# Optimization experiments

Hardware: AMD Instinct MI355X
Metric: run time of the kernel (lower is better)

## Reference

```python
import jax, jax.numpy as jnp
import numpy as np

P, C, NX, NY, NT = 2, 1, 128, 128, 8


def setup_inputs() -> dict:
    key = jax.random.key(0)
    k1, k2 = jax.random.split(key)
    x_5D = jax.random.normal(k1, (P, C, NX, NY, NT), dtype=jnp.float32)
    # per-pixel regularization parameter map (positive)
    lambda_reg = jax.random.uniform(k2, (P, 1, NX, NY, NT), dtype=jnp.float32) * 0.1 + 1e-3
    ten = jnp.asarray(10.0, jnp.float32)  # nn.Parameter init value 10.0
    return {"x_5D": x_5D, "lambda_reg": lambda_reg, "tau": ten, "sigma": ten,
            "theta": ten, "T": 128}


def _grad_G(u):
    # u: (P,1,Nx,Ny,Nt) -> forward finite differences with circular boundary,
    # stacked over the 3 spatial/temporal dims: (P,3,Nx,Ny,Nt)
    v = u[:, 0]
    return jnp.stack([jnp.roll(v, -1, axis=a) - v for a in (1, 2, 3)], axis=1)


def _grad_GH(q):
    # adjoint of _grad_G (negative divergence): (P,3,Nx,Ny,Nt) -> (P,1,Nx,Ny,Nt)
    out = sum(jnp.roll(q[:, d], 1, axis=d + 1) - q[:, d] for d in range(3))
    return out[:, None]


def _clip_act(q, lam):
    # pointwise projection onto [-lam, lam] ball: q * lam / max(lam, |q|)
    return q * lam / jnp.maximum(lam, jnp.abs(q))


def reference(x_5D, lambda_reg, tau, sigma, theta, T):
    dtype = x_5D.dtype
    # L = sqrt(op_norm_AHA^2 + op_norm_GHG^2) = sqrt(1 + 12)
    L = jnp.sqrt(jnp.asarray(13.0, dtype))
    sig = jax.nn.sigmoid(sigma).astype(dtype) / L
    tau_ = jax.nn.sigmoid(tau).astype(dtype) / L
    th = jax.nn.sigmoid(theta).astype(dtype)

    xnoisy = x_5D
    x0 = x_5D
    xbar = x_5D
    p = x_5D
    q = jnp.zeros((x_5D.shape[0], 3) + x_5D.shape[2:], dtype=dtype)

    def step(carry, _):
        x0, xbar, p, q = carry
        p = (p + sig * (xbar - xnoisy)) / (1.0 + sig)
        q = _clip_act(q + sig * _grad_G(xbar), lambda_reg)
        x1 = x0 - tau_ * p - tau_ * _grad_GH(q)
        # updating xbar on the final iteration is dead code in the original
        # (it only skips unused work), so a uniform scan is mathematically identical
        xbar = x1 + th * (x1 - x0)
        return (x1, xbar, p, q), None

    (x1, _, _, _), _ = jax.lax.scan(step, (x0, xbar, p, q), None, length=T)
    return x1
```

## Files before the change

### kernel.cpp

```cpp
#include <hip/hip_runtime.h>
#include <math.h>

#define NSITES (2 * 128 * 128 * 8)
#define NBLK   256
#define NSUP   32
#define TLX    16
#define TLY    24
#define NCOL   (TLX * TLY)
#define NTHR   (NCOL * 2)

union F4 { float4 v; float f[4]; };
union U4 { uint4 v; unsigned w[4]; };

__device__ __forceinline__ unsigned pk_bf2(float lo, float hi) {
    unsigned r;
    asm("v_cvt_pk_bf16_f32 %0, %1, %2" : "=v"(r) : "v"(lo), "v"(hi));
    return r;
}
__device__ __forceinline__ float bf_lo(unsigned p) { return __uint_as_float(p << 16); }
__device__ __forceinline__ float bf_hi(unsigned p) { return __uint_as_float(p & 0xFFFF0000u); }

__device__ __forceinline__ float dpp_swap1(float x) {
    return __int_as_float(
        __builtin_amdgcn_mov_dpp(__float_as_int(x), 0xB1, 0xF, 0xF, true));
}

template <bool FIRST, bool LAST>
__global__ __launch_bounds__(NTHR, 3) void pdhg_col(
    const float* __restrict__ x,
    const float* __restrict__ lam,
    const float* __restrict__ tau_p,
    const float* __restrict__ sigma_p,
    const float* __restrict__ theta_p,
    const unsigned long long* __restrict__ inD1,
    const unsigned long long* __restrict__ inD2,
    unsigned long long* __restrict__ outD1,
    unsigned long long* __restrict__ outD2,
    float* __restrict__ out_final)
{
    __shared__ float4 Lxb[2][NTHR];
    __shared__ uint4  Lqq[2][NTHR];

    const int b  = 32 * (blockIdx.x & 7) + (blockIdx.x >> 3);
    const int pp = b >> 7;
    const int rr = b & 127;
    const int bx = rr >> 3;
    const int by = rr & 7;

    const int t   = threadIdx.x;
    const int tm  = t & 1;
    const int col = t >> 1;
    const int lx  = col / TLY;
    const int ly  = col - lx * TLY;

    const int X  = ((bx << 3) + lx - 4) & 127;
    const int Y  = ((by << 4) + ly - 4) & 127;
    const int Xm = (X + 127) & 127;
    const int Ym = (Y + 127) & 127;

    const int gcol = (pp << 17) | (X << 10) | (Y << 3);
    const int gxm  = (pp << 17) | (Xm << 10) | (Y << 3);
    const int gym  = (pp << 17) | (X << 10) | (Ym << 3);

    const bool comp = (lx >= 1) && (lx < 15) && (ly >= 1) && (ly < 23);

    const float L = 3.605551275463989f;
    const float s_sig = (1.f / (1.f + __expf(-sigma_p[0]))) / L;
    const float s_tau = (1.f / (1.f + __expf(-tau_p[0]))) / L;
    const float s_th  =  1.f / (1.f + __expf(-theta_p[0]));
    const float inv1s = 1.f / (1.f + s_sig);

    const int c4 = (gcol >> 2) + tm;

    float xn[4], lamc[4], lamx[4], lamy[4];
    {
        const float4* x4 = (const float4*)x;
        const float4* l4 = (const float4*)lam;
        if (FIRST || comp) {
            F4 a; a.v = x4[c4];
            #pragma unroll
            for (int j = 0; j < 4; ++j) xn[j] = a.f[j];
        } else {
            #pragma unroll
            for (int j = 0; j < 4; ++j) xn[j] = 0.f;
        }
        if (comp) {
            F4 a;
            a.v = l4[c4];
            #pragma unroll
            for (int j = 0; j < 4; ++j) lamc[j] = a.f[j];
            a.v = l4[(gxm >> 2) + tm];
            #pragma unroll
            for (int j = 0; j < 4; ++j) lamx[j] = a.f[j];
            a.v = l4[(gym >> 2) + tm];
            #pragma unroll
            for (int j = 0; j < 4; ++j) lamy[j] = a.f[j];
        } else {
            #pragma unroll
            for (int j = 0; j < 4; ++j) { lamc[j] = 0.f; lamx[j] = 0.f; lamy[j] = 0.f; }
        }
    }
    const float lamtm = dpp_swap1(lamc[3]);

    float x0[4], p[4], q0[4], q1[4], q2[4], xb[4];
    if (FIRST) {
        #pragma unroll
        for (int j = 0; j < 4; ++j) {
            const float v = xn[j];
            x0[j] = v; p[j] = v; xb[j] = v;
            q0[j] = 0.f; q1[j] = 0.f; q2[j] = 0.f;
        }
    } else {
        const uint4* d1 = (const uint4*)inD1;
        const int base = (gcol >> 1) + 2 * tm;
        #pragma unroll
        for (int k = 0; k < 2; ++k) {
            U4 a; a.v = d1[base + k];
            #pragma unroll
            for (int m = 0; m < 2; ++m) {
                const int j = 2 * k + m;
                const unsigned lo = a.w[2 * m], hi = a.w[2 * m + 1];
                xb[j] = bf_lo(lo); q0[j] = bf_hi(lo);
                q1[j] = bf_lo(hi); q2[j] = bf_hi(hi);
            }
        }
        if (comp) {
            const float4* d2 = (const float4*)inD2;
            #pragma unroll
            for (int k = 0; k < 2; ++k) {
                F4 a; a.v = d2[base + k];
                p[2 * k]     = a.f[0]; x0[2 * k]     = a.f[1];
                p[2 * k + 1] = a.f[2]; x0[2 * k + 1] = a.f[3];
            }
        } else {
            #pragma unroll
            for (int j = 0; j < 4; ++j) { p[j] = 0.f; x0[j] = 0.f; }
        }
    }

    auto clip = [](float v, float l) { return __builtin_amdgcn_fmed3f(v, -l, l); };

    auto substep = [&](const int h) {
        const int pb = h & 1;
        if (lx >= 3 - h && lx < 13 + h && ly >= 3 - h && ly < 21 + h) {
            Lxb[pb][t] = make_float4(xb[0], xb[1], xb[2], xb[3]);
            U4 w;
            w.w[0] = pk_bf2(q0[0], q1[0]); w.w[1] = pk_bf2(q0[1], q1[1]);
            w.w[2] = pk_bf2(q0[2], q1[2]); w.w[3] = pk_bf2(q0[3], q1[3]);
            Lqq[pb][t] = w.v;
        }
        __syncthreads();
        if (lx >= 4 - h && lx < 12 + h && ly >= 4 - h && ly < 20 + h) {
            const float xb_tp = dpp_swap1(xb[0]);
            const float xb_tm = dpp_swap1(xb[3]);
            const float q2_tm = dpp_swap1(q2[3]);
            F4 xp, xm, yp, ym; U4 qx, qy;
            xp.v = Lxb[pb][t + 2 * TLY];
            xm.v = Lxb[pb][t - 2 * TLY];
            yp.v = Lxb[pb][t + 2];
            ym.v = Lxb[pb][t - 2];
            qx.v = Lqq[pb][t - 2 * TLY];
            qy.v = Lqq[pb][t - 2];
            float oxb[4], oq2[4];
            #pragma unroll
            for (int j = 0; j < 4; ++j) { oxb[j] = xb[j]; oq2[j] = q2[j]; }
            #pragma unroll
            for (int j = 0; j < 4; ++j) {
                const float ob   = oxb[j];
                const float xbtp = (j < 3) ? oxb[j + 1] : xb_tp;
                const float xbtm = (j > 0) ? oxb[j - 1] : xb_tm;
                const float q2tm = (j > 0) ? oq2[j - 1] : q2_tm;
                const float lT   = (j > 0) ? lamc[j - 1] : lamtm;
                const float pn  = (p[j] + s_sig * (ob - xn[j])) * inv1s;
                const float q0n = clip(q0[j] + s_sig * (xp.f[j] - ob), lamc[j]);
                const float q1n = clip(q1[j] + s_sig * (yp.f[j] - ob), lamc[j]);
                const float q2n = clip(oq2[j] + s_sig * (xbtp - ob), lamc[j]);
                const float q0m = clip(bf_lo(qx.w[j]) + s_sig * (ob - xm.f[j]), lamx[j]);
                const float q1m = clip(bf_hi(qy.w[j]) + s_sig * (ob - ym.f[j]), lamy[j]);
                const float q2m = clip(q2tm + s_sig * (ob - xbtm), lT);
                const float dv  = (q0m - q0n) + (q1m - q1n) + (q2m - q2n);
                const float x1  = x0[j] - s_tau * (pn + dv);
                xb[j] = x1 + s_th * (x1 - x0[j]);
                x0[j] = x1; p[j] = pn;
                q0[j] = q0n; q1[j] = q1n; q2[j] = q2n;
            }
        }
    };

    substep(3);
    substep(2);
    substep(1);
    substep(0);

    if (lx >= 4 && lx < 12 && ly >= 4 && ly < 20) {
        if (LAST) {
            float4* o4 = (float4*)out_final;
            F4 a;
            a.f[0] = x0[0]; a.f[1] = x0[1]; a.f[2] = x0[2]; a.f[3] = x0[3];
            o4[c4] = a.v;
        } else {
            uint4*  o1 = (uint4*)outD1;
            float4* o2 = (float4*)outD2;
            const int base = (gcol >> 1) + 2 * tm;
            #pragma unroll
            for (int k = 0; k < 2; ++k) {
                U4 w;
                #pragma unroll
                for (int m = 0; m < 2; ++m) {
                    const int j = 2 * k + m;
                    w.w[2 * m]     = pk_bf2(xb[j], q0[j]);
                    w.w[2 * m + 1] = pk_bf2(q1[j], q2[j]);
                }
                o1[base + k] = w.v;
                F4 d;
                d.f[0] = p[2 * k];     d.f[1] = x0[2 * k];
                d.f[2] = p[2 * k + 1]; d.f[3] = x0[2 * k + 1];
                o2[base + k] = d.v;
            }
        }
    }
}

extern "C" void kernel_launch(void* const* d_in, const int* in_sizes, int n_in,
                              void* d_out, int out_size, void* d_ws, size_t ws_size,
                              hipStream_t stream) {
    const float* x   = (const float*)d_in[0];
    const float* lam = (const float*)d_in[1];
    const float* tau = (const float*)d_in[2];
    const float* sig = (const float*)d_in[3];
    const float* th  = (const float*)d_in[4];
    float* out = (float*)d_out;

    unsigned long long* D1 = (unsigned long long*)d_ws;
    unsigned long long* D2 = D1 + 2 * (size_t)NSITES;

    dim3 grid(NBLK), block(NTHR);

    for (int g = 0; g < NSUP; ++g) {
        const size_t si = (size_t)((g + 1) & 1) * NSITES;
        const size_t so = (size_t)(g & 1) * NSITES;
        const unsigned long long *i1 = D1 + si, *i2 = D2 + si;
        unsigned long long *o1 = D1 + so, *o2 = D2 + so;
        if (g == 0) {
            pdhg_col<true, false><<<grid, block, 0, stream>>>(
                x, lam, tau, sig, th, i1, i2, o1, o2, out);
        } else if (g == NSUP - 1) {
            pdhg_col<false, true><<<grid, block, 0, stream>>>(
                x, lam, tau, sig, th, i1, i2, o1, o2, out);
        } else {
            pdhg_col<false, false><<<grid, block, 0, stream>>>(
                x, lam, tau, sig, th, i1, i2, o1, o2, out);
        }
    }
}
```

Baseline: 264.0 us.

## Compute q in a separate phase and share full-precision q via LDS

Each substep is split into two phases with an extra barrier. The first phase updates q0/q1/q2 from neighbour xbar and stores q0/q1 to shared memory in fp32. The second phase reads the upstream q neighbours to form the divergence, instead of recomputing the neighbour clipped q values from bf16-packed q and neighbour lambda maps. This removes the redundant neighbour q recomputation, the bf16 packing, and the extra lambda loads, at the cost of a second __syncthreads per substep, more LDS traffic, and single-buffered LDS.

```diff
diff --git a/kernel.cpp b/kernel.cpp
--- a/kernel.cpp
+++ b/kernel.cpp
@@ -38,8 +38,9 @@
     unsigned long long* __restrict__ outD2,
     float* __restrict__ out_final)
 {
-    __shared__ float4 Lxb[2][NTHR];
-    __shared__ uint4  Lqq[2][NTHR];
+    __shared__ float4 Lxb[NTHR];
+    __shared__ float4 Lq0[NTHR];
+    __shared__ float4 Lq1[NTHR];
 
     const int b  = 32 * (blockIdx.x & 7) + (blockIdx.x >> 3);
     const int pp = b >> 7;
@@ -55,12 +56,8 @@
 
     const int X  = ((bx << 3) + lx - 4) & 127;
     const int Y  = ((by << 4) + ly - 4) & 127;
-    const int Xm = (X + 127) & 127;
-    const int Ym = (Y + 127) & 127;
 
     const int gcol = (pp << 17) | (X << 10) | (Y << 3);
-    const int gxm  = (pp << 17) | (Xm << 10) | (Y << 3);
-    const int gym  = (pp << 17) | (X << 10) | (Ym << 3);
 
     const bool comp = (lx >= 1) && (lx < 15) && (ly >= 1) && (ly < 23);
 
@@ -72,35 +69,18 @@
 
     const int c4 = (gcol >> 2) + tm;
 
-    float xn[4], lamc[4], lamx[4], lamy[4];
+    float xn[4], lamc[4];
     {
         const float4* x4 = (const float4*)x;
         const float4* l4 = (const float4*)lam;
-        if (FIRST || comp) {
-            F4 a; a.v = x4[c4];
-            #pragma unroll
-            for (int j = 0; j < 4; ++j) xn[j] = a.f[j];
-        } else {
-            #pragma unroll
-            for (int j = 0; j < 4; ++j) xn[j] = 0.f;
-        }
-        if (comp) {
-            F4 a;
-            a.v = l4[c4];
-            #pragma unroll
-            for (int j = 0; j < 4; ++j) lamc[j] = a.f[j];
-            a.v = l4[(gxm >> 2) + tm];
-            #pragma unroll
-            for (int j = 0; j < 4; ++j) lamx[j] = a.f[j];
-            a.v = l4[(gym >> 2) + tm];
-            #pragma unroll
-            for (int j = 0; j < 4; ++j) lamy[j] = a.f[j];
-        } else {
-            #pragma unroll
-            for (int j = 0; j < 4; ++j) { lamc[j] = 0.f; lamx[j] = 0.f; lamy[j] = 0.f; }
-        }
-    }
-    const float lamtm = dpp_swap1(lamc[3]);
+        F4 a;
+        a.v = x4[c4];
+        #pragma unroll
+        for (int j = 0; j < 4; ++j) xn[j] = a.f[j];
+        a.v = l4[c4];
+        #pragma unroll
+        for (int j = 0; j < 4; ++j) lamc[j] = a.f[j];
+    }
 
     float x0[4], p[4], q0[4], q1[4], q2[4], xb[4];
     if (FIRST) {
@@ -141,48 +121,43 @@
     auto clip = [](float v, float l) { return __builtin_amdgcn_fmed3f(v, -l, l); };
 
     auto substep = [&](const int h) {
-        const int pb = h & 1;
         if (lx >= 3 - h && lx < 13 + h && ly >= 3 - h && ly < 21 + h) {
-            Lxb[pb][t] = make_float4(xb[0], xb[1], xb[2], xb[3]);
-            U4 w;
-            w.w[0] = pk_bf2(q0[0], q1[0]); w.w[1] = pk_bf2(q0[1], q1[1]);
-            w.w[2] = pk_bf2(q0[2], q1[2]); w.w[3] = pk_bf2(q0[3], q1[3]);
-            Lqq[pb][t] = w.v;
+            Lxb[t] = make_float4(xb[0], xb[1], xb[2], xb[3]);
+        }
+        __syncthreads();
+        const bool inQ = (lx >= 3 - h) && (lx < 12 + h) &&
+                         (ly >= 3 - h) && (ly < 20 + h);
+        if (inQ) {
+            F4 xp, yp;
+            xp.v = Lxb[t + 2 * TLY];
+            yp.v = Lxb[t + 2];
+            const float xb_tp = dpp_swap1(xb[0]);
+            #pragma unroll
+            for (int j = 0; j < 4; ++j) {
+                const float ob   = xb[j];
+                const float xbtp = (j < 3) ? xb[j + 1] : xb_tp;
+                q0[j] = clip(q0[j] + s_sig * (xp.f[j] - ob), lamc[j]);
+                q1[j] = clip(q1[j] + s_sig * (yp.f[j] - ob), lamc[j]);
+                q2[j] = clip(q2[j] + s_sig * (xbtp   - ob), lamc[j]);
+            }
+            Lq0[t] = make_float4(q0[0], q0[1], q0[2], q0[3]);
+            Lq1[t] = make_float4(q1[0], q1[1], q1[2], q1[3]);
         }
         __syncthreads();
         if (lx >= 4 - h && lx < 12 + h && ly >= 4 - h && ly < 20 + h) {
-            const float xb_tp = dpp_swap1(xb[0]);
-            const float xb_tm = dpp_swap1(xb[3]);
+            F4 qx, qy;
+            qx.v = Lq0[t - 2 * TLY];
+            qy.v = Lq1[t - 2];
             const float q2_tm = dpp_swap1(q2[3]);
-            F4 xp, xm, yp, ym; U4 qx, qy;
-            xp.v = Lxb[pb][t + 2 * TLY];
-            xm.v = Lxb[pb][t - 2 * TLY];
-            yp.v = Lxb[pb][t + 2];
-            ym.v = Lxb[pb][t - 2];
-            qx.v = Lqq[pb][t - 2 * TLY];
-            qy.v = Lqq[pb][t - 2];
-            float oxb[4], oq2[4];
-            #pragma unroll
-            for (int j = 0; j < 4; ++j) { oxb[j] = xb[j]; oq2[j] = q2[j]; }
             #pragma unroll
             for (int j = 0; j < 4; ++j) {
-                const float ob   = oxb[j];
-                const float xbtp = (j < 3) ? oxb[j + 1] : xb_tp;
-                const float xbtm = (j > 0) ? oxb[j - 1] : xb_tm;
-                const float q2tm = (j > 0) ? oq2[j - 1] : q2_tm;
-                const float lT   = (j > 0) ? lamc[j - 1] : lamtm;
+                const float ob  = xb[j];
                 const float pn  = (p[j] + s_sig * (ob - xn[j])) * inv1s;
-                const float q0n = clip(q0[j] + s_sig * (xp.f[j] - ob), lamc[j]);
-                const float q1n = clip(q1[j] + s_sig * (yp.f[j] - ob), lamc[j]);
-                const float q2n = clip(oq2[j] + s_sig * (xbtp - ob), lamc[j]);
-                const float q0m = clip(bf_lo(qx.w[j]) + s_sig * (ob - xm.f[j]), lamx[j]);
-                const float q1m = clip(bf_hi(qy.w[j]) + s_sig * (ob - ym.f[j]), lamy[j]);
-                const float q2m = clip(q2tm + s_sig * (ob - xbtm), lT);
-                const float dv  = (q0m - q0n) + (q1m - q1n) + (q2m - q2n);
+                const float q2m = (j > 0) ? q2[j - 1] : q2_tm;
+                const float dv  = (qx.f[j] - q0[j]) + (qy.f[j] - q1[j]) + (q2m - q2[j]);
                 const float x1  = x0[j] - s_tau * (pn + dv);
                 xb[j] = x1 + s_th * (x1 - x0[j]);
                 x0[j] = x1; p[j] = pn;
-                q0[j] = q0n; q1[j] = q1n; q2[j] = q2n;
             }
         }
     };
```

New measurement: 255.4 us. 1.03x faster.
